# Optimization experiments

Hardware: AMD Instinct MI355X
Metric: run time of the kernel (lower is better)

## Reference

```python
import jax, jax.numpy as jnp
import numpy as np

B, S, L = 32, 512, 64
START, STOP, PAD = 61, 62, 63
NEG = -10000.0


def setup_inputs() -> dict:
    key = jax.random.key(0)
    k1, k2, k3, k4 = jax.random.split(key, 4)
    encoder_scores = jax.random.normal(k1, (B, S, L), dtype=jnp.float32)
    transition = jax.random.normal(k2, (L, L), dtype=jnp.float32)
    # constrained transitions, as in __init__
    transition = (transition.at[:, START].set(NEG)
                            .at[STOP, :].set(NEG)
                            .at[:, PAD].set(NEG)
                            .at[PAD, :].set(NEG))
    word_seq_lens = jax.random.randint(k3, (B,), S // 2, S + 1)  # in [S/2, S]
    tags = jax.random.randint(k4, (B, S), 0, START)  # valid non-special labels
    mask = jnp.arange(S)[None, :] < word_seq_lens[:, None]
    return {"encoder_scores": encoder_scores, "transition": transition,
            "word_seq_lens": word_seq_lens, "tags": tags, "mask": mask}


def reference(encoder_scores, transition, word_seq_lens, tags, mask):
    # all_scores[b,s,i,j] = transition[i,j] + encoder_scores[b,s,j]  (B,S,L,L)
    all_scores = transition[None, None, :, :] + encoder_scores[:, :, None, :]

    # ---- forward algorithm (partition function) ----
    alpha0 = all_scores[:, 0, START, :]  # (B,L)

    def step(a_prev, s_t):  # a_prev (B,L), s_t (B,L,L)
        a = jax.nn.logsumexp(a_prev[:, :, None] + s_t, axis=1)
        return a, a

    _, alphas_rest = jax.lax.scan(step, alpha0,
                                  jnp.swapaxes(all_scores[:, 1:], 0, 1))
    alphas = jnp.concatenate([alpha0[:, None, :],
                              jnp.swapaxes(alphas_rest, 0, 1)], axis=1)  # (B,S,L)
    last_alpha = jnp.take_along_axis(
        alphas, (word_seq_lens - 1)[:, None, None], axis=1)[:, 0, :]  # (B,L)
    last_alpha = last_alpha + transition[:, STOP][None, :]
    unlabeled = jax.nn.logsumexp(last_alpha, axis=1)  # (B,)

    # ---- gold-sequence score ----
    # cur[b,s,i] = all_scores[b,s,i,tags[b,s]]
    cur = jnp.take_along_axis(all_scores, tags[:, :, None, None], axis=3)[..., 0]  # (B,S,L)
    mid = jnp.take_along_axis(cur[:, 1:, :], tags[:, :-1, None], axis=2)[..., 0]  # (B,S-1)
    begin = cur[:, 0, START]  # (B,)
    end_ids = jnp.take_along_axis(tags, (word_seq_lens - 1)[:, None], axis=1)[:, 0]
    end_sc = transition[end_ids, STOP]  # (B,)
    labeled = begin + end_sc + jnp.sum(mid * mask[:, 1:].astype(mid.dtype), axis=1)
    return unlabeled, labeled
```

## Files before the change

### kernel.cpp

```cpp
#include <hip/hip_runtime.h>

#define BB 32
#define SS 512
#define LL 64
#define TSTART 61
#define TSTOP 62
#define NSEG 16
#define SEGLEN 32
#define QPAD 68

typedef short short8 __attribute__((ext_vector_type(8)));
typedef float floatx4 __attribute__((ext_vector_type(4)));

union S8 { int i[4]; short8 v; };

__device__ inline unsigned bf16_rne(float x) {
    unsigned u = __float_as_uint(x);
    u += 0x7fffu + ((u >> 16) & 1u);
    return u >> 16;
}
__device__ inline int pack_bf16(float a, float b) {
    return (int)(bf16_rne(a) | (bf16_rne(b) << 16));
}

__global__ __launch_bounds__(64) void crf_seg_kernel(
    const float* __restrict__ enc, const float* __restrict__ Tr,
    const int* __restrict__ lens, const int* __restrict__ tags,
    float* __restrict__ wsQ, float* __restrict__ wsS,
    float* __restrict__ out)
{
    const int blk = blockIdx.x;
    if (blk >= BB * NSEG * 4) {
        const int b = blk - BB * NSEG * 4;
        const int tid = threadIdx.x;
        const int len = lens[b];
        const int* tg = tags + b * SS;
        const float* eb = enc + b * (SS * LL);
        float acc = 0.f;
        for (int t = 1 + tid; t < len; t += 64) {
            int curt = tg[t], prevt = tg[t - 1];
            acc += Tr[prevt * LL + curt] + eb[t * LL + curt];
        }
        #pragma unroll
        for (int off = 32; off; off >>= 1) acc += __shfl_xor(acc, off);
        if (tid == 0) {
            int t0 = tg[0], te = tg[len - 1];
            acc += Tr[TSTART * LL + t0] + eb[t0];
            acc += Tr[te * LL + TSTOP];
            out[BB + b] = acc;
        }
        return;
    }

    const int lane = threadIdx.x;
    const int b = blk >> 6;
    const int s = (blk >> 2) & 15;
    const int g = blk & 3;
    const int len = lens[b];
    const int q = lane >> 4;
    const int lcol = lane & 15;
    const float* eb = enc + b * (SS * LL);
    const int tlo = SEGLEN * s + 1;
    const int Teff = min(max(len - tlo, 0), SEGLEN);

    float* qdst = wsQ + (size_t)(b * NSEG + s) * 4096;

    if (Teff <= 0) {
        #pragma unroll
        for (int u = 0; u < 4; ++u) {
            int r0 = 16 * q + 4 * u;
            float4 v;
            v.x = (r0 + 0 == 16 * g + lcol) ? 1.f : 0.f;
            v.y = (r0 + 1 == 16 * g + lcol) ? 1.f : 0.f;
            v.z = (r0 + 2 == 16 * g + lcol) ? 1.f : 0.f;
            v.w = (r0 + 3 == 16 * g + lcol) ? 1.f : 0.f;
            *(float4*)(qdst + (16 * g + lcol) * 64 + r0) = v;
        }
        if (lane == 0) wsS[(b * NSEG + s) * 4 + g] = 0.f;
        return;
    }

    __shared__ __align__(16) float QT[16 * QPAD];
    __shared__ __align__(16) float W32[32 * 64];

    short8 Afr[4][2];
    #pragma unroll
    for (int mt = 0; mt < 4; ++mt)
        #pragma unroll
        for (int c2 = 0; c2 < 2; ++c2) {
            float av[8];
            #pragma unroll
            for (int idx = 0; idx < 8; ++idx) {
                int kk = 32 * c2 + 8 * q + idx;
                int mm = 16 * mt + lcol;
                av[idx] = __expf(Tr[kk * LL + mm]) * 0.0078125f;
            }
            S8 u;
            #pragma unroll
            for (int w2 = 0; w2 < 4; ++w2) u.i[w2] = pack_bf16(av[2 * w2], av[2 * w2 + 1]);
            Afr[mt][c2] = u.v;
        }

    {
        const float* trow = Tr + (16 * g + lcol) * LL;
        #pragma unroll
        for (int u = 0; u < 4; ++u) {
            float4 tv = *(const float4*)(trow + 16 * q + 4 * u);
            float4 ev;
            ev.x = __expf(tv.x) * 0.0078125f;
            ev.y = __expf(tv.y) * 0.0078125f;
            ev.z = __expf(tv.z) * 0.0078125f;
            ev.w = __expf(tv.w) * 0.0078125f;
            *(float4*)(QT + lcol * QPAD + 16 * q + 4 * u) = ev;
        }
    }

    float lg = 0.0f;
    float ecur[8], enxt[8];
    #pragma unroll
    for (int k = 0; k < 8; ++k) ecur[k] = eb[min(tlo + k, SS - 1) * LL + lane];
    #pragma unroll
    for (int k = 0; k < 8; ++k) enxt[k] = eb[min(tlo + 8 + k, SS - 1) * LL + lane];

    for (int cc = 0; cc < 4; ++cc) {
        #pragma unroll
        for (int k = 0; k < 8; ++k) W32[(8 * cc + k) * 64 + lane] = __expf(ecur[k]);
        float epre[8];
        #pragma unroll
        for (int k = 0; k < 8; ++k) epre[k] = eb[min(tlo + 8 * (cc + 2) + k, SS - 1) * LL + lane];

        #pragma unroll
        for (int k = 0; k < 8; ++k) {
            const int i = 8 * cc + k + 2;
            if (i <= Teff) {
                const int wloc = 8 * cc + k;
                float4 qv[2][2], wv[2][2];
                #pragma unroll
                for (int c2 = 0; c2 < 2; ++c2)
                    #pragma unroll
                    for (int h = 0; h < 2; ++h) {
                        qv[c2][h] = *(const float4*)(QT + lcol * QPAD + 32 * c2 + 8 * q + 4 * h);
                        wv[c2][h] = *(const float4*)(W32 + wloc * 64 + 32 * c2 + 8 * q + 4 * h);
                    }
                short8 Bfr[2];
                #pragma unroll
                for (int c2 = 0; c2 < 2; ++c2) {
                    float bv[8];
                    bv[0] = qv[c2][0].x * wv[c2][0].x;  bv[1] = qv[c2][0].y * wv[c2][0].y;
                    bv[2] = qv[c2][0].z * wv[c2][0].z;  bv[3] = qv[c2][0].w * wv[c2][0].w;
                    bv[4] = qv[c2][1].x * wv[c2][1].x;  bv[5] = qv[c2][1].y * wv[c2][1].y;
                    bv[6] = qv[c2][1].z * wv[c2][1].z;  bv[7] = qv[c2][1].w * wv[c2][1].w;
                    S8 u;
                    #pragma unroll
                    for (int w2 = 0; w2 < 4; ++w2)
                        u.i[w2] = pack_bf16(bv[2 * w2], bv[2 * w2 + 1]);
                    Bfr[c2] = u.v;
                }
                float ov[4][4];
                #pragma unroll
                for (int mt = 0; mt < 4; ++mt) {
                    floatx4 z = {0.f, 0.f, 0.f, 0.f};
                    z = __builtin_amdgcn_mfma_f32_16x16x32_bf16(Afr[mt][0], Bfr[0], z, 0, 0, 0);
                    z = __builtin_amdgcn_mfma_f32_16x16x32_bf16(Afr[mt][1], Bfr[1], z, 0, 0, 0);
                    ov[mt][0] = z[0]; ov[mt][1] = z[1]; ov[mt][2] = z[2]; ov[mt][3] = z[3];
                }
                if (k == 7) {
                    float mx = ov[0][0];
                    #pragma unroll
                    for (int mt = 0; mt < 4; ++mt)
                        #pragma unroll
                        for (int r = 0; r < 4; ++r) mx = fmaxf(mx, ov[mt][r]);
                    #pragma unroll
                    for (int off = 32; off; off >>= 1) mx = fmaxf(mx, __shfl_xor(mx, off));
                    lg += __logf(mx);
                    float rmx = 1.0f / mx;
                    #pragma unroll
                    for (int mt = 0; mt < 4; ++mt)
                        #pragma unroll
                        for (int r = 0; r < 4; ++r) ov[mt][r] *= rmx;
                }
                #pragma unroll
                for (int mt = 0; mt < 4; ++mt) {
                    float4 sv = make_float4(ov[mt][0], ov[mt][1], ov[mt][2], ov[mt][3]);
                    *(float4*)(QT + lcol * QPAD + 16 * mt + 4 * q) = sv;
                }
            }
        }
        #pragma unroll
        for (int k = 0; k < 8; ++k) { ecur[k] = enxt[k]; enxt[k] = epre[k]; }
    }

    const float* wl = W32 + (Teff - 1) * 64;
    #pragma unroll
    for (int u = 0; u < 4; ++u) {
        int r0 = 16 * q + 4 * u;
        float4 mv = *(const float4*)(QT + lcol * QPAD + r0);
        float4 wv = *(const float4*)(wl + r0);
        float4 o = make_float4(mv.x * wv.x, mv.y * wv.y, mv.z * wv.z, mv.w * wv.w);
        *(float4*)(qdst + (16 * g + lcol) * 64 + r0) = o;
    }
    if (lane == 0) wsS[(b * NSEG + s) * 4 + g] = lg;
}

__global__ __launch_bounds__(64) void crf_combine_kernel(
    const float* __restrict__ enc, const float* __restrict__ Tr,
    const int* __restrict__ lens,
    const float* __restrict__ wsQ, const float* __restrict__ wsS,
    float* __restrict__ out)
{
    const int b = blockIdx.x;
    const int j = threadIdx.x;
    const int len = lens[b];
    const float* qb = wsQ + (size_t)b * NSEG * 4096;

    float alpha0 = Tr[TSTART * LL + j] + enc[b * (SS * LL) + j];
    float m = alpha0;
    #pragma unroll
    for (int off = 32; off; off >>= 1) m = fmaxf(m, __shfl_xor(m, off));
    float a = __expf(alpha0 - m);
    float logscale = m;

    float myscale = wsS[b * (NSEG * 4) + j];

    float A[64], Bv[64];
    #pragma unroll
    for (int c = 0; c < 64; ++c) A[c] = qb[c * 64 + j];

    auto step = [&](int s, float (&cur)[64]) {
        float l0 = __shfl(myscale, 4 * s + 0);
        float l1 = __shfl(myscale, 4 * s + 1);
        float l2 = __shfl(myscale, 4 * s + 2);
        float l3 = __shfl(myscale, 4 * s + 3);
        float lmax = fmaxf(fmaxf(l0, l1), fmaxf(l2, l3));
        int grp = j >> 4;
        float lgg = (grp == 0) ? l0 : (grp == 1) ? l1 : (grp == 2) ? l2 : l3;
        float at = a * __expf(lgg - lmax);
        int ai = __float_as_int(at);
        float s0 = 0.f, s1 = 0.f, s2 = 0.f, s3 = 0.f;
        #pragma unroll
        for (int c = 0; c < 16; ++c) {
            s0 = fmaf(__int_as_float(__builtin_amdgcn_readlane(ai, 4 * c + 0)), cur[4 * c + 0], s0);
            s1 = fmaf(__int_as_float(__builtin_amdgcn_readlane(ai, 4 * c + 1)), cur[4 * c + 1], s1);
            s2 = fmaf(__int_as_float(__builtin_amdgcn_readlane(ai, 4 * c + 2)), cur[4 * c + 2], s2);
            s3 = fmaf(__int_as_float(__builtin_amdgcn_readlane(ai, 4 * c + 3)), cur[4 * c + 3], s3);
        }
        float an = ((s0 + s1) + (s2 + s3));
        float mx = an;
        #pragma unroll
        for (int off = 32; off; off >>= 1) mx = fmaxf(mx, __shfl_xor(mx, off));
        a = an * (1.0f / mx);
        logscale += lmax + __logf(mx);
    };

    for (int s = 0; s < 16; s += 2) {
        const float* q1 = qb + (size_t)min(s + 1, NSEG - 1) * 4096;
        #pragma unroll
        for (int c = 0; c < 64; ++c) Bv[c] = q1[c * 64 + j];
        step(s, A);
        const float* q2 = qb + (size_t)min(s + 2, NSEG - 1) * 4096;
        #pragma unroll
        for (int c = 0; c < 64; ++c) A[c] = q2[c * 64 + j];
        step(s + 1, Bv);
    }

    float f = a * __expf(Tr[j * LL + TSTOP]);
    float ssum = f;
    #pragma unroll
    for (int off = 32; off; off >>= 1) ssum += __shfl_xor(ssum, off);
    if (j == 0) {
        const float LN2x7 = 7.0f * 0.69314718055994530942f;
        out[b] = logscale + (float)(len - 1) * LN2x7 + __logf(ssum);
    }
}

__global__ __launch_bounds__(256) void crf_kernel_fb(
    const float* __restrict__ enc, const float* __restrict__ Tr,
    const int* __restrict__ lens, const int* __restrict__ tags,
    float* __restrict__ out)
{
    if (blockIdx.x < BB) {
        const int tid = threadIdx.x;
        if (tid >= 64) return;
        const int b = blockIdx.x;
        const int j = tid;
        const int len = lens[b];
        const float* eb = enc + b * (SS * LL);
        float Ecol[LL];
        #pragma unroll
        for (int i = 0; i < LL; ++i) Ecol[i] = __expf(Tr[i * LL + j]) * 0.0078125f;
        float alpha0 = Tr[TSTART * LL + j] + eb[j];
        float m = alpha0;
        #pragma unroll
        for (int off = 32; off; off >>= 1) m = fmaxf(m, __shfl_xor(m, off));
        float a = __expf(alpha0 - m);
        float logscale = m;
        float ecur[4], enext[4];
        #pragma unroll
        for (int k = 0; k < 4; ++k) ecur[k] = eb[k * LL + j];
        #pragma unroll
        for (int k = 0; k < 4; ++k) enext[k] = eb[(4 + k) * LL + j];
        const int nchunk = (len + 3) >> 2;
        for (int c = 0; c < nchunk; ++c) {
            const int cpre = (c + 2 < 128) ? (c + 2) : 127;
            float efar[4];
            #pragma unroll
            for (int k = 0; k < 4; ++k) efar[k] = eb[(4 * cpre + k) * LL + j];
            #pragma unroll
            for (int k = 0; k < 4; ++k) {
                const int t = 4 * c + k;
                if (t >= 1 && t < len) {
                    const float w = __expf(ecur[k]);
                    const int ai = __float_as_int(a);
                    float s0 = 0.f, s1 = 0.f, s2 = 0.f, s3 = 0.f;
                    #pragma unroll
                    for (int qq = 0; qq < 16; ++qq) {
                        s0 = fmaf(__int_as_float(__builtin_amdgcn_readlane(ai, 4 * qq + 0)), Ecol[4 * qq + 0], s0);
                        s1 = fmaf(__int_as_float(__builtin_amdgcn_readlane(ai, 4 * qq + 1)), Ecol[4 * qq + 1], s1);
                        s2 = fmaf(__int_as_float(__builtin_amdgcn_readlane(ai, 4 * qq + 2)), Ecol[4 * qq + 2], s2);
                        s3 = fmaf(__int_as_float(__builtin_amdgcn_readlane(ai, 4 * qq + 3)), Ecol[4 * qq + 3], s3);
                    }
                    a = ((s0 + s1) + (s2 + s3)) * w;
                    if ((t & 7) == 7) {
                        float mm = a;
                        #pragma unroll
                        for (int off = 32; off; off >>= 1) mm = fmaxf(mm, __shfl_xor(mm, off));
                        logscale += __logf(mm);
                        a = a * (1.0f / mm);
                    }
                }
            }
            #pragma unroll
            for (int k = 0; k < 4; ++k) { ecur[k] = enext[k]; enext[k] = efar[k]; }
        }
        float f = a * __expf(Tr[j * LL + TSTOP]);
        float ssum = f;
        #pragma unroll
        for (int off = 32; off; off >>= 1) ssum += __shfl_xor(ssum, off);
        if (j == 0) {
            const float LN2x7 = 7.0f * 0.69314718055994530942f;
            out[b] = logscale + (float)(len - 1) * LN2x7 + __logf(ssum);
        }
    } else {
        const int b = blockIdx.x - BB;
        const int tid = threadIdx.x;
        const int len = lens[b];
        const int* tg = tags + b * SS;
        const float* eb = enc + b * (SS * LL);
        float acc = 0.f;
        for (int t = 1 + tid; t < len; t += 256) {
            int curt = tg[t], prevt = tg[t - 1];
            acc += Tr[prevt * LL + curt] + eb[t * LL + curt];
        }
        #pragma unroll
        for (int off = 32; off; off >>= 1) acc += __shfl_xor(acc, off);
        __shared__ float red[4];
        if ((tid & 63) == 0) red[tid >> 6] = acc;
        __syncthreads();
        if (tid == 0) {
            float tot = (red[0] + red[1]) + (red[2] + red[3]);
            int t0 = tg[0], te = tg[len - 1];
            tot += Tr[TSTART * LL + t0] + eb[t0];
            tot += Tr[te * LL + TSTOP];
            out[BB + b] = tot;
        }
    }
}

extern "C" void kernel_launch(void* const* d_in, const int* in_sizes, int n_in,
                              void* d_out, int out_size, void* d_ws, size_t ws_size,
                              hipStream_t stream) {
    const float* enc  = (const float*)d_in[0];
    const float* Tr   = (const float*)d_in[1];
    const int*   lens = (const int*)d_in[2];
    const int*   tags = (const int*)d_in[3];
    float* out = (float*)d_out;

    const size_t needQ = (size_t)BB * NSEG * 4096 * sizeof(float);
    const size_t needS = (size_t)BB * NSEG * 4 * sizeof(float);
    if (ws_size >= needQ + needS) {
        float* wsQ = (float*)d_ws;
        float* wsS = (float*)((char*)d_ws + needQ);
        crf_seg_kernel<<<BB * NSEG * 4 + BB, 64, 0, stream>>>(enc, Tr, lens, tags, wsQ, wsS, out);
        crf_combine_kernel<<<BB, 64, 0, stream>>>(enc, Tr, lens, wsQ, wsS, out);
    } else {
        crf_kernel_fb<<<2 * BB, 256, 0, stream>>>(enc, Tr, lens, tags, out);
    }
}
```

Before: 98.55 us.

## Fuse segment and combine kernels via per-batch atomic last-block-done counter

Merges the segment-product kernel and the combine kernel into one launch. Each segment block fences and atomically bumps a per-batch counter, and the last of the 64 blocks for a batch runs the combine step. This removes a kernel launch boundary and lets combine for early-finishing batches overlap with other segment work. In exchange it adds a memset launch, atomics and fences, and the serial combine now runs inside a single 64-thread block with register pressure from the fused code.

```diff
diff --git a/kernel.cpp b/kernel.cpp
--- a/kernel.cpp
+++ b/kernel.cpp
@@ -23,193 +23,11 @@
     return (int)(bf16_rne(a) | (bf16_rne(b) << 16));
 }
 
-__global__ __launch_bounds__(64) void crf_seg_kernel(
-    const float* __restrict__ enc, const float* __restrict__ Tr,
-    const int* __restrict__ lens, const int* __restrict__ tags,
-    float* __restrict__ wsQ, float* __restrict__ wsS,
-    float* __restrict__ out)
+__device__ void combine_batch(int b, int j, const float* __restrict__ enc,
+                              const float* __restrict__ Tr, const int* __restrict__ lens,
+                              const float* __restrict__ wsQ, const float* __restrict__ wsS,
+                              float* __restrict__ out)
 {
-    const int blk = blockIdx.x;
-    if (blk >= BB * NSEG * 4) {
-        const int b = blk - BB * NSEG * 4;
-        const int tid = threadIdx.x;
-        const int len = lens[b];
-        const int* tg = tags + b * SS;
-        const float* eb = enc + b * (SS * LL);
-        float acc = 0.f;
-        for (int t = 1 + tid; t < len; t += 64) {
-            int curt = tg[t], prevt = tg[t - 1];
-            acc += Tr[prevt * LL + curt] + eb[t * LL + curt];
-        }
-        #pragma unroll
-        for (int off = 32; off; off >>= 1) acc += __shfl_xor(acc, off);
-        if (tid == 0) {
-            int t0 = tg[0], te = tg[len - 1];
-            acc += Tr[TSTART * LL + t0] + eb[t0];
-            acc += Tr[te * LL + TSTOP];
-            out[BB + b] = acc;
-        }
-        return;
-    }
-
-    const int lane = threadIdx.x;
-    const int b = blk >> 6;
-    const int s = (blk >> 2) & 15;
-    const int g = blk & 3;
-    const int len = lens[b];
-    const int q = lane >> 4;
-    const int lcol = lane & 15;
-    const float* eb = enc + b * (SS * LL);
-    const int tlo = SEGLEN * s + 1;
-    const int Teff = min(max(len - tlo, 0), SEGLEN);
-
-    float* qdst = wsQ + (size_t)(b * NSEG + s) * 4096;
-
-    if (Teff <= 0) {
-        #pragma unroll
-        for (int u = 0; u < 4; ++u) {
-            int r0 = 16 * q + 4 * u;
-            float4 v;
-            v.x = (r0 + 0 == 16 * g + lcol) ? 1.f : 0.f;
-            v.y = (r0 + 1 == 16 * g + lcol) ? 1.f : 0.f;
-            v.z = (r0 + 2 == 16 * g + lcol) ? 1.f : 0.f;
-            v.w = (r0 + 3 == 16 * g + lcol) ? 1.f : 0.f;
-            *(float4*)(qdst + (16 * g + lcol) * 64 + r0) = v;
-        }
-        if (lane == 0) wsS[(b * NSEG + s) * 4 + g] = 0.f;
-        return;
-    }
-
-    __shared__ __align__(16) float QT[16 * QPAD];
-    __shared__ __align__(16) float W32[32 * 64];
-
-    short8 Afr[4][2];
-    #pragma unroll
-    for (int mt = 0; mt < 4; ++mt)
-        #pragma unroll
-        for (int c2 = 0; c2 < 2; ++c2) {
-            float av[8];
-            #pragma unroll
-            for (int idx = 0; idx < 8; ++idx) {
-                int kk = 32 * c2 + 8 * q + idx;
-                int mm = 16 * mt + lcol;
-                av[idx] = __expf(Tr[kk * LL + mm]) * 0.0078125f;
-            }
-            S8 u;
-            #pragma unroll
-            for (int w2 = 0; w2 < 4; ++w2) u.i[w2] = pack_bf16(av[2 * w2], av[2 * w2 + 1]);
-            Afr[mt][c2] = u.v;
-        }
-
-    {
-        const float* trow = Tr + (16 * g + lcol) * LL;
-        #pragma unroll
-        for (int u = 0; u < 4; ++u) {
-            float4 tv = *(const float4*)(trow + 16 * q + 4 * u);
-            float4 ev;
-            ev.x = __expf(tv.x) * 0.0078125f;
-            ev.y = __expf(tv.y) * 0.0078125f;
-            ev.z = __expf(tv.z) * 0.0078125f;
-            ev.w = __expf(tv.w) * 0.0078125f;
-            *(float4*)(QT + lcol * QPAD + 16 * q + 4 * u) = ev;
-        }
-    }
-
-    float lg = 0.0f;
-    float ecur[8], enxt[8];
-    #pragma unroll
-    for (int k = 0; k < 8; ++k) ecur[k] = eb[min(tlo + k, SS - 1) * LL + lane];
-    #pragma unroll
-    for (int k = 0; k < 8; ++k) enxt[k] = eb[min(tlo + 8 + k, SS - 1) * LL + lane];
-
-    for (int cc = 0; cc < 4; ++cc) {
-        #pragma unroll
-        for (int k = 0; k < 8; ++k) W32[(8 * cc + k) * 64 + lane] = __expf(ecur[k]);
-        float epre[8];
-        #pragma unroll
-        for (int k = 0; k < 8; ++k) epre[k] = eb[min(tlo + 8 * (cc + 2) + k, SS - 1) * LL + lane];
-
-        #pragma unroll
-        for (int k = 0; k < 8; ++k) {
-            const int i = 8 * cc + k + 2;
-            if (i <= Teff) {
-                const int wloc = 8 * cc + k;
-                float4 qv[2][2], wv[2][2];
-                #pragma unroll
-                for (int c2 = 0; c2 < 2; ++c2)
-                    #pragma unroll
-                    for (int h = 0; h < 2; ++h) {
-                        qv[c2][h] = *(const float4*)(QT + lcol * QPAD + 32 * c2 + 8 * q + 4 * h);
-                        wv[c2][h] = *(const float4*)(W32 + wloc * 64 + 32 * c2 + 8 * q + 4 * h);
-                    }
-                short8 Bfr[2];
-                #pragma unroll
-                for (int c2 = 0; c2 < 2; ++c2) {
-                    float bv[8];
-                    bv[0] = qv[c2][0].x * wv[c2][0].x;  bv[1] = qv[c2][0].y * wv[c2][0].y;
-                    bv[2] = qv[c2][0].z * wv[c2][0].z;  bv[3] = qv[c2][0].w * wv[c2][0].w;
-                    bv[4] = qv[c2][1].x * wv[c2][1].x;  bv[5] = qv[c2][1].y * wv[c2][1].y;
-                    bv[6] = qv[c2][1].z * wv[c2][1].z;  bv[7] = qv[c2][1].w * wv[c2][1].w;
-                    S8 u;
-                    #pragma unroll
-                    for (int w2 = 0; w2 < 4; ++w2)
-                        u.i[w2] = pack_bf16(bv[2 * w2], bv[2 * w2 + 1]);
-                    Bfr[c2] = u.v;
-                }
-                float ov[4][4];
-                #pragma unroll
-                for (int mt = 0; mt < 4; ++mt) {
-                    floatx4 z = {0.f, 0.f, 0.f, 0.f};
-                    z = __builtin_amdgcn_mfma_f32_16x16x32_bf16(Afr[mt][0], Bfr[0], z, 0, 0, 0);
-                    z = __builtin_amdgcn_mfma_f32_16x16x32_bf16(Afr[mt][1], Bfr[1], z, 0, 0, 0);
-                    ov[mt][0] = z[0]; ov[mt][1] = z[1]; ov[mt][2] = z[2]; ov[mt][3] = z[3];
-                }
-                if (k == 7) {
-                    float mx = ov[0][0];
-                    #pragma unroll
-                    for (int mt = 0; mt < 4; ++mt)
-                        #pragma unroll
-                        for (int r = 0; r < 4; ++r) mx = fmaxf(mx, ov[mt][r]);
-                    #pragma unroll
-                    for (int off = 32; off; off >>= 1) mx = fmaxf(mx, __shfl_xor(mx, off));
-                    lg += __logf(mx);
-                    float rmx = 1.0f / mx;
-                    #pragma unroll
-                    for (int mt = 0; mt < 4; ++mt)
-                        #pragma unroll
-                        for (int r = 0; r < 4; ++r) ov[mt][r] *= rmx;
-                }
-                #pragma unroll
-                for (int mt = 0; mt < 4; ++mt) {
-                    float4 sv = make_float4(ov[mt][0], ov[mt][1], ov[mt][2], ov[mt][3]);
-                    *(float4*)(QT + lcol * QPAD + 16 * mt + 4 * q) = sv;
-                }
-            }
-        }
-        #pragma unroll
-        for (int k = 0; k < 8; ++k) { ecur[k] = enxt[k]; enxt[k] = epre[k]; }
-    }
-
-    const float* wl = W32 + (Teff - 1) * 64;
-    #pragma unroll
-    for (int u = 0; u < 4; ++u) {
-        int r0 = 16 * q + 4 * u;
-        float4 mv = *(const float4*)(QT + lcol * QPAD + r0);
-        float4 wv = *(const float4*)(wl + r0);
-        float4 o = make_float4(mv.x * wv.x, mv.y * wv.y, mv.z * wv.z, mv.w * wv.w);
-        *(float4*)(qdst + (16 * g + lcol) * 64 + r0) = o;
-    }
-    if (lane == 0) wsS[(b * NSEG + s) * 4 + g] = lg;
-}
-
-__global__ __launch_bounds__(64) void crf_combine_kernel(
-    const float* __restrict__ enc, const float* __restrict__ Tr,
-    const int* __restrict__ lens,
-    const float* __restrict__ wsQ, const float* __restrict__ wsS,
-    float* __restrict__ out)
-{
-    const int b = blockIdx.x;
-    const int j = threadIdx.x;
     const int len = lens[b];
     const float* qb = wsQ + (size_t)b * NSEG * 4096;
 
@@ -270,6 +88,193 @@
     if (j == 0) {
         const float LN2x7 = 7.0f * 0.69314718055994530942f;
         out[b] = logscale + (float)(len - 1) * LN2x7 + __logf(ssum);
+    }
+}
+
+__global__ __launch_bounds__(64) void crf_fused_kernel(
+    const float* __restrict__ enc, const float* __restrict__ Tr,
+    const int* __restrict__ lens, const int* __restrict__ tags,
+    float* __restrict__ wsQ, float* __restrict__ wsS, int* __restrict__ cnt,
+    float* __restrict__ out)
+{
+    const int blk = blockIdx.x;
+    const int lane = threadIdx.x;
+
+    if (blk >= BB * NSEG * 4) {
+        const int b = blk - BB * NSEG * 4;
+        const int len = lens[b];
+        const int* tg = tags + b * SS;
+        const float* eb = enc + b * (SS * LL);
+        float acc = 0.f;
+        for (int t = 1 + lane; t < len; t += 64) {
+            int curt = tg[t], prevt = tg[t - 1];
+            acc += Tr[prevt * LL + curt] + eb[t * LL + curt];
+        }
+        #pragma unroll
+        for (int off = 32; off; off >>= 1) acc += __shfl_xor(acc, off);
+        if (lane == 0) {
+            int t0 = tg[0], te = tg[len - 1];
+            acc += Tr[TSTART * LL + t0] + eb[t0];
+            acc += Tr[te * LL + TSTOP];
+            out[BB + b] = acc;
+        }
+        return;
+    }
+
+    const int b = blk >> 6;
+    const int s = (blk >> 2) & 15;
+    const int g = blk & 3;
+    const int len = lens[b];
+    const int q = lane >> 4;
+    const int lcol = lane & 15;
+    const float* eb = enc + b * (SS * LL);
+    const int tlo = SEGLEN * s + 1;
+    const int Teff = min(max(len - tlo, 0), SEGLEN);
+
+    float* qdst = wsQ + (size_t)(b * NSEG + s) * 4096;
+
+    if (Teff <= 0) {
+        #pragma unroll
+        for (int u = 0; u < 4; ++u) {
+            int r0 = 16 * q + 4 * u;
+            float4 v;
+            v.x = (r0 + 0 == 16 * g + lcol) ? 1.f : 0.f;
+            v.y = (r0 + 1 == 16 * g + lcol) ? 1.f : 0.f;
+            v.z = (r0 + 2 == 16 * g + lcol) ? 1.f : 0.f;
+            v.w = (r0 + 3 == 16 * g + lcol) ? 1.f : 0.f;
+            *(float4*)(qdst + (16 * g + lcol) * 64 + r0) = v;
+        }
+        if (lane == 0) wsS[(b * NSEG + s) * 4 + g] = 0.f;
+    } else {
+        __shared__ __align__(16) float QT[16 * QPAD];
+        __shared__ __align__(16) float W32[32 * 64];
+
+        short8 Afr[4][2];
+        #pragma unroll
+        for (int mt = 0; mt < 4; ++mt)
+            #pragma unroll
+            for (int c2 = 0; c2 < 2; ++c2) {
+                float av[8];
+                #pragma unroll
+                for (int idx = 0; idx < 8; ++idx) {
+                    int kk = 32 * c2 + 8 * q + idx;
+                    int mm = 16 * mt + lcol;
+                    av[idx] = __expf(Tr[kk * LL + mm]) * 0.0078125f;
+                }
+                S8 u;
+                #pragma unroll
+                for (int w2 = 0; w2 < 4; ++w2) u.i[w2] = pack_bf16(av[2 * w2], av[2 * w2 + 1]);
+                Afr[mt][c2] = u.v;
+            }
+
+        {
+            const float* trow = Tr + (16 * g + lcol) * LL;
+            #pragma unroll
+            for (int u = 0; u < 4; ++u) {
+                float4 tv = *(const float4*)(trow + 16 * q + 4 * u);
+                float4 ev;
+                ev.x = __expf(tv.x) * 0.0078125f;
+                ev.y = __expf(tv.y) * 0.0078125f;
+                ev.z = __expf(tv.z) * 0.0078125f;
+                ev.w = __expf(tv.w) * 0.0078125f;
+                *(float4*)(QT + lcol * QPAD + 16 * q + 4 * u) = ev;
+            }
+        }
+
+        float lg = 0.0f;
+        float ecur[8], enxt[8];
+        #pragma unroll
+        for (int k = 0; k < 8; ++k) ecur[k] = eb[min(tlo + k, SS - 1) * LL + lane];
+        #pragma unroll
+        for (int k = 0; k < 8; ++k) enxt[k] = eb[min(tlo + 8 + k, SS - 1) * LL + lane];
+
+        for (int cc = 0; cc < 4; ++cc) {
+            #pragma unroll
+            for (int k = 0; k < 8; ++k) W32[(8 * cc + k) * 64 + lane] = __expf(ecur[k]);
+            float epre[8];
+            #pragma unroll
+            for (int k = 0; k < 8; ++k) epre[k] = eb[min(tlo + 8 * (cc + 2) + k, SS - 1) * LL + lane];
+
+            #pragma unroll
+            for (int k = 0; k < 8; ++k) {
+                const int i = 8 * cc + k + 2;
+                if (i <= Teff) {
+                    const int wloc = 8 * cc + k;
+                    float4 qv[2][2], wv[2][2];
+                    #pragma unroll
+                    for (int c2 = 0; c2 < 2; ++c2)
+                        #pragma unroll
+                        for (int h = 0; h < 2; ++h) {
+                            qv[c2][h] = *(const float4*)(QT + lcol * QPAD + 32 * c2 + 8 * q + 4 * h);
+                            wv[c2][h] = *(const float4*)(W32 + wloc * 64 + 32 * c2 + 8 * q + 4 * h);
+                        }
+                    short8 Bfr[2];
+                    #pragma unroll
+                    for (int c2 = 0; c2 < 2; ++c2) {
+                        float bv[8];
+                        bv[0] = qv[c2][0].x * wv[c2][0].x;  bv[1] = qv[c2][0].y * wv[c2][0].y;
+                        bv[2] = qv[c2][0].z * wv[c2][0].z;  bv[3] = qv[c2][0].w * wv[c2][0].w;
+                        bv[4] = qv[c2][1].x * wv[c2][1].x;  bv[5] = qv[c2][1].y * wv[c2][1].y;
+                        bv[6] = qv[c2][1].z * wv[c2][1].z;  bv[7] = qv[c2][1].w * wv[c2][1].w;
+                        S8 u;
+                        #pragma unroll
+                        for (int w2 = 0; w2 < 4; ++w2)
+                            u.i[w2] = pack_bf16(bv[2 * w2], bv[2 * w2 + 1]);
+                        Bfr[c2] = u.v;
+                    }
+                    float ov[4][4];
+                    #pragma unroll
+                    for (int mt = 0; mt < 4; ++mt) {
+                        floatx4 z = {0.f, 0.f, 0.f, 0.f};
+                        z = __builtin_amdgcn_mfma_f32_16x16x32_bf16(Afr[mt][0], Bfr[0], z, 0, 0, 0);
+                        z = __builtin_amdgcn_mfma_f32_16x16x32_bf16(Afr[mt][1], Bfr[1], z, 0, 0, 0);
+                        ov[mt][0] = z[0]; ov[mt][1] = z[1]; ov[mt][2] = z[2]; ov[mt][3] = z[3];
+                    }
+                    if (k == 7) {
+                        float mx = ov[0][0];
+                        #pragma unroll
+                        for (int mt = 0; mt < 4; ++mt)
+                            #pragma unroll
+                            for (int r = 0; r < 4; ++r) mx = fmaxf(mx, ov[mt][r]);
+                        #pragma unroll
+                        for (int off = 32; off; off >>= 1) mx = fmaxf(mx, __shfl_xor(mx, off));
+                        lg += __logf(mx);
+                        float rmx = 1.0f / mx;
+                        #pragma unroll
+                        for (int mt = 0; mt < 4; ++mt)
+                            #pragma unroll
+                            for (int r = 0; r < 4; ++r) ov[mt][r] *= rmx;
+                    }
+                    #pragma unroll
+                    for (int mt = 0; mt < 4; ++mt) {
+                        float4 sv = make_float4(ov[mt][0], ov[mt][1], ov[mt][2], ov[mt][3]);
+                        *(float4*)(QT + lcol * QPAD + 16 * mt + 4 * q) = sv;
+                    }
+                }
+            }
+            #pragma unroll
+            for (int k = 0; k < 8; ++k) { ecur[k] = enxt[k]; enxt[k] = epre[k]; }
+        }
+
+        const float* wl = W32 + (Teff - 1) * 64;
+        #pragma unroll
+        for (int u = 0; u < 4; ++u) {
+            int r0 = 16 * q + 4 * u;
+            float4 mv = *(const float4*)(QT + lcol * QPAD + r0);
+            float4 wv = *(const float4*)(wl + r0);
+            float4 o = make_float4(mv.x * wv.x, mv.y * wv.y, mv.z * wv.z, mv.w * wv.w);
+            *(float4*)(qdst + (16 * g + lcol) * 64 + r0) = o;
+        }
+        if (lane == 0) wsS[(b * NSEG + s) * 4 + g] = lg;
+    }
+
+    __threadfence();
+    int old = 0;
+    if (lane == 0) old = atomicAdd(&cnt[b], 1);
+    old = __shfl(old, 0);
+    if (old == 63) {
+        __threadfence();
+        combine_batch(b, lane, enc, Tr, lens, wsQ, wsS, out);
     }
 }
 
@@ -377,11 +382,13 @@
 
     const size_t needQ = (size_t)BB * NSEG * 4096 * sizeof(float);
     const size_t needS = (size_t)BB * NSEG * 4 * sizeof(float);
-    if (ws_size >= needQ + needS) {
+    const size_t needC = (size_t)BB * sizeof(int);
+    if (ws_size >= needQ + needS + needC) {
         float* wsQ = (float*)d_ws;
         float* wsS = (float*)((char*)d_ws + needQ);
-        crf_seg_kernel<<<BB * NSEG * 4 + BB, 64, 0, stream>>>(enc, Tr, lens, tags, wsQ, wsS, out);
-        crf_combine_kernel<<<BB, 64, 0, stream>>>(enc, Tr, lens, wsQ, wsS, out);
+        int*   cnt = (int*)((char*)d_ws + needQ + needS);
+        hipMemsetAsync(cnt, 0, needC, stream);
+        crf_fused_kernel<<<BB * NSEG * 4 + BB, 64, 0, stream>>>(enc, Tr, lens, tags, wsQ, wsS, cnt, out);
     } else {
         crf_kernel_fb<<<2 * BB, 256, 0, stream>>>(enc, Tr, lens, tags, out);
     }
```

Measured after the change: 168.0 us. +70.5%, slower.

## Split sequence into 32 shorter segments and skip empty segments in combine

Applied to the files above, without the earlier changes.

Halves the segment length and doubles the segment count, so each of the now twice as many wavefronts runs a 16-step serial matrix product chain instead of 32. Segments past the sequence length no longer write identity matrices; the combine kernel instead stops at the last valid segment, loads segment matrices in 16-row chunks with a rolling prefetch, and reads two scale vectors. The cost is a combine stage with twice as many serial 64x64 steps for full-length sequences, and more per-block setup overhead relative to the work each block does.

```diff
diff --git a/kernel.cpp b/kernel.cpp
--- a/kernel.cpp
+++ b/kernel.cpp
@@ -5,8 +5,8 @@
 #define LL 64
 #define TSTART 61
 #define TSTOP 62
-#define NSEG 16
-#define SEGLEN 32
+#define NSEG 32
+#define SEGLEN 16
 #define QPAD 68
 
 typedef short short8 __attribute__((ext_vector_type(8)));
@@ -30,20 +30,21 @@
     float* __restrict__ out)
 {
     const int blk = blockIdx.x;
+    const int lane = threadIdx.x;
+
     if (blk >= BB * NSEG * 4) {
         const int b = blk - BB * NSEG * 4;
-        const int tid = threadIdx.x;
         const int len = lens[b];
         const int* tg = tags + b * SS;
         const float* eb = enc + b * (SS * LL);
         float acc = 0.f;
-        for (int t = 1 + tid; t < len; t += 64) {
+        for (int t = 1 + lane; t < len; t += 64) {
             int curt = tg[t], prevt = tg[t - 1];
             acc += Tr[prevt * LL + curt] + eb[t * LL + curt];
         }
         #pragma unroll
         for (int off = 32; off; off >>= 1) acc += __shfl_xor(acc, off);
-        if (tid == 0) {
+        if (lane == 0) {
             int t0 = tg[0], te = tg[len - 1];
             acc += Tr[TSTART * LL + t0] + eb[t0];
             acc += Tr[te * LL + TSTOP];
@@ -52,36 +53,25 @@
         return;
     }
 
-    const int lane = threadIdx.x;
-    const int b = blk >> 6;
-    const int s = (blk >> 2) & 15;
+    const int b = blk >> 7;
+    const int s = (blk >> 2) & 31;
     const int g = blk & 3;
     const int len = lens[b];
+    const int tlo = SEGLEN * s + 1;
+    const int Teff = min(len - tlo, SEGLEN);
+    if (Teff <= 0) return;
+
     const int q = lane >> 4;
     const int lcol = lane & 15;
     const float* eb = enc + b * (SS * LL);
-    const int tlo = SEGLEN * s + 1;
-    const int Teff = min(max(len - tlo, 0), SEGLEN);
-
     float* qdst = wsQ + (size_t)(b * NSEG + s) * 4096;
 
-    if (Teff <= 0) {
-        #pragma unroll
-        for (int u = 0; u < 4; ++u) {
-            int r0 = 16 * q + 4 * u;
-            float4 v;
-            v.x = (r0 + 0 == 16 * g + lcol) ? 1.f : 0.f;
-            v.y = (r0 + 1 == 16 * g + lcol) ? 1.f : 0.f;
-            v.z = (r0 + 2 == 16 * g + lcol) ? 1.f : 0.f;
-            v.w = (r0 + 3 == 16 * g + lcol) ? 1.f : 0.f;
-            *(float4*)(qdst + (16 * g + lcol) * 64 + r0) = v;
-        }
-        if (lane == 0) wsS[(b * NSEG + s) * 4 + g] = 0.f;
-        return;
-    }
-
     __shared__ __align__(16) float QT[16 * QPAD];
-    __shared__ __align__(16) float W32[32 * 64];
+    __shared__ __align__(16) float W16[16 * 64];
+
+    float ev[16];
+    #pragma unroll
+    for (int k = 0; k < 16; ++k) ev[k] = eb[min(tlo + k, SS - 1) * LL + lane];
 
     short8 Afr[4][2];
     #pragma unroll
@@ -106,29 +96,21 @@
         #pragma unroll
         for (int u = 0; u < 4; ++u) {
             float4 tv = *(const float4*)(trow + 16 * q + 4 * u);
-            float4 ev;
-            ev.x = __expf(tv.x) * 0.0078125f;
-            ev.y = __expf(tv.y) * 0.0078125f;
-            ev.z = __expf(tv.z) * 0.0078125f;
-            ev.w = __expf(tv.w) * 0.0078125f;
-            *(float4*)(QT + lcol * QPAD + 16 * q + 4 * u) = ev;
-        }
-    }
+            float4 evv;
+            evv.x = __expf(tv.x) * 0.0078125f;
+            evv.y = __expf(tv.y) * 0.0078125f;
+            evv.z = __expf(tv.z) * 0.0078125f;
+            evv.w = __expf(tv.w) * 0.0078125f;
+            *(float4*)(QT + lcol * QPAD + 16 * q + 4 * u) = evv;
+        }
+    }
+
+    #pragma unroll
+    for (int k = 0; k < 16; ++k) W16[k * 64 + lane] = __expf(ev[k]);
 
     float lg = 0.0f;
-    float ecur[8], enxt[8];
-    #pragma unroll
-    for (int k = 0; k < 8; ++k) ecur[k] = eb[min(tlo + k, SS - 1) * LL + lane];
-    #pragma unroll
-    for (int k = 0; k < 8; ++k) enxt[k] = eb[min(tlo + 8 + k, SS - 1) * LL + lane];
-
-    for (int cc = 0; cc < 4; ++cc) {
-        #pragma unroll
-        for (int k = 0; k < 8; ++k) W32[(8 * cc + k) * 64 + lane] = __expf(ecur[k]);
-        float epre[8];
-        #pragma unroll
-        for (int k = 0; k < 8; ++k) epre[k] = eb[min(tlo + 8 * (cc + 2) + k, SS - 1) * LL + lane];
-
+    #pragma unroll
+    for (int cc = 0; cc < 2; ++cc) {
         #pragma unroll
         for (int k = 0; k < 8; ++k) {
             const int i = 8 * cc + k + 2;
@@ -140,7 +122,7 @@
                     #pragma unroll
                     for (int h = 0; h < 2; ++h) {
                         qv[c2][h] = *(const float4*)(QT + lcol * QPAD + 32 * c2 + 8 * q + 4 * h);
-                        wv[c2][h] = *(const float4*)(W32 + wloc * 64 + 32 * c2 + 8 * q + 4 * h);
+                        wv[c2][h] = *(const float4*)(W16 + wloc * 64 + 32 * c2 + 8 * q + 4 * h);
                     }
                 short8 Bfr[2];
                 #pragma unroll
@@ -164,7 +146,7 @@
                     z = __builtin_amdgcn_mfma_f32_16x16x32_bf16(Afr[mt][1], Bfr[1], z, 0, 0, 0);
                     ov[mt][0] = z[0]; ov[mt][1] = z[1]; ov[mt][2] = z[2]; ov[mt][3] = z[3];
                 }
-                if (k == 7) {
+                if (cc == 0 && k == 7) {
                     float mx = ov[0][0];
                     #pragma unroll
                     for (int mt = 0; mt < 4; ++mt)
@@ -186,11 +168,9 @@
                 }
             }
         }
-        #pragma unroll
-        for (int k = 0; k < 8; ++k) { ecur[k] = enxt[k]; enxt[k] = epre[k]; }
-    }
-
-    const float* wl = W32 + (Teff - 1) * 64;
+    }
+
+    const float* wl = W16 + (Teff - 1) * 64;
     #pragma unroll
     for (int u = 0; u < 4; ++u) {
         int r0 = 16 * q + 4 * u;
@@ -211,6 +191,7 @@
     const int b = blockIdx.x;
     const int j = threadIdx.x;
     const int len = lens[b];
+    const int smax = (len - 2) / SEGLEN + 1;
     const float* qb = wsQ + (size_t)b * NSEG * 4096;
 
     float alpha0 = Tr[TSTART * LL + j] + enc[b * (SS * LL) + j];
@@ -220,47 +201,56 @@
     float a = __expf(alpha0 - m);
     float logscale = m;
 
-    float myscale = wsS[b * (NSEG * 4) + j];
-
-    float A[64], Bv[64];
-    #pragma unroll
-    for (int c = 0; c < 64; ++c) A[c] = qb[c * 64 + j];
-
-    auto step = [&](int s, float (&cur)[64]) {
-        float l0 = __shfl(myscale, 4 * s + 0);
-        float l1 = __shfl(myscale, 4 * s + 1);
-        float l2 = __shfl(myscale, 4 * s + 2);
-        float l3 = __shfl(myscale, 4 * s + 3);
+    float sc0 = wsS[b * (NSEG * 4) + j];
+    float sc1 = wsS[b * (NSEG * 4) + 64 + j];
+
+    float B0[16], B1[16], B2[16], B3[16];
+    auto load16 = [&](float (&Bf)[16], int chunk) {
+        const float* p = qb + (size_t)chunk * 1024 + j;
+        #pragma unroll
+        for (int u = 0; u < 16; ++u) Bf[u] = p[u * 64];
+    };
+    load16(B0, 0); load16(B1, 1); load16(B2, 2);
+
+    const int CMAX = 4 * NSEG - 1;
+    for (int s = 0; s < smax; ++s) {
+        float l0, l1, l2, l3;
+        if (s < 16) {
+            l0 = __shfl(sc0, 4 * s + 0); l1 = __shfl(sc0, 4 * s + 1);
+            l2 = __shfl(sc0, 4 * s + 2); l3 = __shfl(sc0, 4 * s + 3);
+        } else {
+            int e = 4 * (s - 16);
+            l0 = __shfl(sc1, e + 0); l1 = __shfl(sc1, e + 1);
+            l2 = __shfl(sc1, e + 2); l3 = __shfl(sc1, e + 3);
+        }
         float lmax = fmaxf(fmaxf(l0, l1), fmaxf(l2, l3));
         int grp = j >> 4;
         float lgg = (grp == 0) ? l0 : (grp == 1) ? l1 : (grp == 2) ? l2 : l3;
         float at = a * __expf(lgg - lmax);
         int ai = __float_as_int(at);
-        float s0 = 0.f, s1 = 0.f, s2 = 0.f, s3 = 0.f;
-        #pragma unroll
-        for (int c = 0; c < 16; ++c) {
-            s0 = fmaf(__int_as_float(__builtin_amdgcn_readlane(ai, 4 * c + 0)), cur[4 * c + 0], s0);
-            s1 = fmaf(__int_as_float(__builtin_amdgcn_readlane(ai, 4 * c + 1)), cur[4 * c + 1], s1);
-            s2 = fmaf(__int_as_float(__builtin_amdgcn_readlane(ai, 4 * c + 2)), cur[4 * c + 2], s2);
-            s3 = fmaf(__int_as_float(__builtin_amdgcn_readlane(ai, 4 * c + 3)), cur[4 * c + 3], s3);
-        }
-        float an = ((s0 + s1) + (s2 + s3));
+
+        float a0 = 0.f, a1 = 0.f, a2 = 0.f, a3 = 0.f;
+        const int sb = 4 * s;
+        #define MAC16(BUF, BASE)                                                        \
+            { _Pragma("unroll")                                                         \
+              for (int u = 0; u < 16; u += 4) {                                         \
+                a0 = fmaf(__int_as_float(__builtin_amdgcn_readlane(ai, BASE + u + 0)), BUF[u + 0], a0); \
+                a1 = fmaf(__int_as_float(__builtin_amdgcn_readlane(ai, BASE + u + 1)), BUF[u + 1], a1); \
+                a2 = fmaf(__int_as_float(__builtin_amdgcn_readlane(ai, BASE + u + 2)), BUF[u + 2], a2); \
+                a3 = fmaf(__int_as_float(__builtin_amdgcn_readlane(ai, BASE + u + 3)), BUF[u + 3], a3); \
+              } }
+        load16(B3, min(sb + 3, CMAX));  MAC16(B0, 0);
+        load16(B0, min(sb + 4, CMAX));  MAC16(B1, 16);
+        load16(B1, min(sb + 5, CMAX));  MAC16(B2, 32);
+        load16(B2, min(sb + 6, CMAX));  MAC16(B3, 48);
+        #undef MAC16
+
+        float an = (a0 + a1) + (a2 + a3);
         float mx = an;
         #pragma unroll
         for (int off = 32; off; off >>= 1) mx = fmaxf(mx, __shfl_xor(mx, off));
         a = an * (1.0f / mx);
         logscale += lmax + __logf(mx);
-    };
-
-    for (int s = 0; s < 16; s += 2) {
-        const float* q1 = qb + (size_t)min(s + 1, NSEG - 1) * 4096;
-        #pragma unroll
-        for (int c = 0; c < 64; ++c) Bv[c] = q1[c * 64 + j];
-        step(s, A);
-        const float* q2 = qb + (size_t)min(s + 2, NSEG - 1) * 4096;
-        #pragma unroll
-        for (int c = 0; c < 64; ++c) A[c] = q2[c * 64 + j];
-        step(s + 1, Bv);
     }
 
     float f = a * __expf(Tr[j * LL + TSTOP]);
```

Measured after the change: 114.9 us. +16.6%, slower.
